# Performance work log

Measured on AMD Instinct MI355X. Metric: run time of the kernel, lower is better.

Reference implementation:

```python
import jax, jax.numpy as jnp
import numpy as np
import math

NUM_HEADS = 8
DIM = 512

def setup_inputs() -> dict:
    key = jax.random.key(0)
    ks = jax.random.split(key, 10)
    t, b, a, f, d = 32, 64, 16, 128, DIM
    inp = {
        "q_embeds": jax.random.normal(ks[0], (t, b, a, d), dtype=jnp.float32),
        "context_embeds": jax.random.normal(ks[1], (t, f, b, d), dtype=jnp.float32),
        "attn_mask": jnp.ones((b, f), dtype=jnp.int32),
        "Wq": jax.random.normal(ks[2], (d, d), dtype=jnp.float32) / math.sqrt(d),
        "bq": jnp.zeros((d,), dtype=jnp.float32),
        "Wk": jax.random.normal(ks[3], (d, d), dtype=jnp.float32) / math.sqrt(d),
        "bk": jnp.zeros((d,), dtype=jnp.float32),
        "Wv": jax.random.normal(ks[4], (d, d), dtype=jnp.float32) / math.sqrt(d),
        "bv": jnp.zeros((d,), dtype=jnp.float32),
        "Wo": jax.random.normal(ks[5], (d, d), dtype=jnp.float32) / math.sqrt(d),
        "bo": jnp.zeros((d,), dtype=jnp.float32),
    }
    return inp

def reference(q_embeds, context_embeds, attn_mask, Wq, bq, Wk, bk, Wv, bv, Wo, bo):
    t, b, a, d = q_embeds.shape
    H = NUM_HEADS
    hd = d // H
    # q: (t,b,a,d) -> (t,b,H,hd,a)
    q = (q_embeds @ Wq.T + bq).reshape(t, b, a, H, hd).transpose(0, 1, 3, 4, 2)
    f = context_embeds.shape[1]
    # video_embeds: (t,f,b,d) -> (t,b,f,d)
    video_embeds = context_embeds.transpose(0, 2, 1, 3)
    # k_proj on (t,f,b,d) then raw reshape to (t,b,f,H,hd) -- faithful to torch .reshape
    k = (context_embeds @ Wk.T + bk).reshape(t, b, f, H, hd).transpose(0, 1, 3, 2, 4)  # (t,b,H,f,hd)
    v = (video_embeds @ Wv.T + bv).reshape(t, b, f, H, hd).transpose(0, 1, 3, 4, 2)   # (t,b,H,hd,f)
    logits = (k @ q) / math.sqrt(hd)  # (t,b,H,f,a)
    mask = attn_mask[None, :, None, :, None]  # (1,b,1,f,1)
    logits = jnp.where(mask == 0, jnp.float32(-1e9), logits)
    weights = jax.nn.softmax(logits, axis=-2)  # softmax over f
    attn = v @ weights  # (t,b,H,hd,a)
    attn = attn.transpose(0, 1, 4, 2, 3).reshape(t, b, a, d)
    o = attn @ Wo.T + bo  # (t,b,a,d)
    return (o.transpose(0, 2, 1, 3), weights)
```

## Files before the change

### kernel.cpp

```cpp
#include <hip/hip_runtime.h>
#include <hip/hip_bf16.h>

typedef __attribute__((ext_vector_type(8))) short short8;
typedef __attribute__((ext_vector_type(4))) float f32x4;

#define NT 32
#define NB 64
#define NA 16
#define NF 128
#define DT 512
#define NH 8
#define NHD 64

__device__ __forceinline__ unsigned short f2b(float f) {
  return __bfloat16_as_ushort(__float2bfloat16(f));
}
__device__ __forceinline__ float b2f(unsigned short u) {
  union { unsigned u; float f; } c; c.u = ((unsigned)u) << 16;
  return c.f;
}
__device__ __forceinline__ unsigned cvt2(float a, float b) {
  return (unsigned)f2b(a) | ((unsigned)f2b(b) << 16);
}

__device__ __forceinline__ void gload16(const void* g, void* l) {
  __builtin_amdgcn_global_load_lds(
      (const __attribute__((address_space(1))) void*)g,
      (__attribute__((address_space(3))) void*)l, 16, 0, 0);
}

#define BAR() asm volatile("s_barrier" ::: "memory")

__global__ __launch_bounds__(256) void cast_kernel(const float* __restrict__ src,
                                                   unsigned short* __restrict__ dst) {
  long i = ((long)blockIdx.x * 256 + threadIdx.x) * 8;
  float4 v0 = *(const float4*)(src + i);
  float4 v1 = *(const float4*)(src + i + 4);
  uint4 o;
  o.x = cvt2(v0.x, v0.y);
  o.y = cvt2(v0.z, v0.w);
  o.z = cvt2(v1.x, v1.y);
  o.w = cvt2(v1.z, v1.w);
  *(uint4*)(dst + i) = o;
}

template <int MODE, int NCB>
__global__ __launch_bounds__(512, 4) void gemm_f32a(const float* __restrict__ A,
                                                    const unsigned short* __restrict__ Bg,
                                                    const float* __restrict__ bias0,
                                                    const float* __restrict__ bias1,
                                                    unsigned short* __restrict__ C0,
                                                    unsigned short* __restrict__ C1) {
  __shared__ __align__(16) float Asf[2][128 * 32];
  __shared__ __align__(16) unsigned short Bsb[2][256 * 32];
  const int tid = threadIdx.x;
  const int lane = tid & 63;
  const int l4 = lane & 15, lg = lane >> 4;
  const int w = tid >> 6;
  const int wm = w >> 2, wn = w & 3;

  const int nwg = gridDim.x;
  const int bid = blockIdx.x;
  const int swz = (bid & 7) * (nwg >> 3) + (bid >> 3);
  const long rowTile = swz >> NCB;
  const int colTile = swz & ((1 << NCB) - 1);

  const int sA = (tid & 7) ^ ((tid >> 3) & 7);
  const float* Agl = A + (rowTile * 128 + (tid >> 3)) * 512L + sA * 4;
  const int sB = (tid & 3) ^ ((tid >> 3) & 3);
  const unsigned short* Bgl = Bg + ((long)colTile * 256 + (tid >> 2)) * 512L + sB * 8;

  auto stage = [&](int s, int kc) {
    gload16(Agl + kc, &Asf[s][w * 256]);
    gload16(Agl + 64 * 512L + kc, &Asf[s][2048 + w * 256]);
    gload16(Bgl + kc, &Bsb[s][w * 512]);
    gload16(Bgl + 128 * 512L + kc, &Bsb[s][4096 + w * 512]);
  };

  const f32x4 zero = {0.f, 0.f, 0.f, 0.f};
  f32x4 acc[4][4];
#pragma unroll
  for (int i = 0; i < 4; i++)
#pragma unroll
    for (int j = 0; j < 4; j++) acc[i][j] = zero;

  const int chA = (l4 & 7);
  const int chB = ((l4 >> 1) & 3);

  stage(0, 0);

#pragma unroll 1
  for (int T = 0; T < 16; T++) {
    const int s = T & 1;
    BAR();
    if (T < 15) {
      stage(s ^ 1, (T + 1) * 32);
      asm volatile("s_waitcnt vmcnt(4)" ::: "memory");
    } else {
      asm volatile("s_waitcnt vmcnt(0)" ::: "memory");
    }
    BAR();
    short8 bf[4];
#pragma unroll
    for (int n = 0; n < 4; n++) {
      int rb = wn * 64 + n * 16 + l4;
      bf[n] = *(const short8*)&Bsb[s][rb * 32 + (lg ^ chB) * 8];
    }
    short8 af[4];
#pragma unroll
    for (int m = 0; m < 4; m++) {
      int ra = wm * 64 + m * 16 + l4;
      int c0 = (lg * 2) ^ chA;
      f32x4 p0 = *(const f32x4*)&Asf[s][ra * 32 + c0 * 4];
      f32x4 p1 = *(const f32x4*)&Asf[s][ra * 32 + (c0 ^ 1) * 4];
      union { unsigned u[4]; short8 s8; } cv;
      cv.u[0] = cvt2(p0[0], p0[1]);
      cv.u[1] = cvt2(p0[2], p0[3]);
      cv.u[2] = cvt2(p1[0], p1[1]);
      cv.u[3] = cvt2(p1[2], p1[3]);
      af[m] = cv.s8;
    }
    __builtin_amdgcn_s_setprio(1);
#pragma unroll
    for (int m = 0; m < 4; m++)
#pragma unroll
      for (int n = 0; n < 4; n++)
        acc[m][n] = __builtin_amdgcn_mfma_f32_16x16x32_bf16(af[m], bf[n], acc[m][n], 0, 0, 0);
    __builtin_amdgcn_s_setprio(0);
  }

  const long rowBase = rowTile * 128 + wm * 64;

  if constexpr (MODE == 0) {
    if (colTile < 2) {
#pragma unroll
      for (int n = 0; n < 4; n++) {
        int gCol = colTile * 256 + wn * 64 + n * 16 + l4;
        float bs = bias0[gCol];
#pragma unroll
        for (int m = 0; m < 4; m++)
#pragma unroll
          for (int r = 0; r < 4; r++) {
            long gRow = rowBase + m * 16 + lg * 4 + r;
            C0[gRow * 512 + gCol] = f2b(acc[m][n][r] + bs);
          }
      }
    } else {
#pragma unroll
      for (int n = 0; n < 4; n++) {
        int gCol = (colTile - 2) * 256 + wn * 64 + n * 16 + l4;
        float bs = bias1[gCol];
#pragma unroll
        for (int m = 0; m < 4; m++)
#pragma unroll
          for (int r = 0; r < 4; r++) {
            long gRow = rowBase + m * 16 + lg * 4 + r;
            long rr = gRow & 8191;
            long vrow = (gRow - rr) + ((rr & 63) << 7) + (rr >> 6);
            C1[vrow * 512 + gCol] = f2b(acc[m][n][r] + bs);
          }
      }
    }
  } else {
#pragma unroll
    for (int n = 0; n < 4; n++) {
      int gCol = colTile * 256 + wn * 64 + n * 16 + l4;
      float bs = bias0[gCol];
#pragma unroll
      for (int m = 0; m < 4; m++)
#pragma unroll
        for (int r = 0; r < 4; r++) {
          long gRow = rowBase + m * 16 + lg * 4 + r;
          C0[gRow * 512 + gCol] = f2b(acc[m][n][r] + bs);
        }
    }
  }
}

__global__ __launch_bounds__(256) void gemm_o(const unsigned short* __restrict__ A,
                                              const unsigned short* __restrict__ Bg,
                                              const float* __restrict__ bias0,
                                              float* __restrict__ C) {
  __shared__ __align__(16) unsigned short As[128 * 32];
  __shared__ __align__(16) unsigned short Bs[128 * 32];
  const int tid = threadIdx.x;
  const int lane = tid & 63;
  const int l4 = lane & 15, lg = lane >> 4;
  const int w = tid >> 6;
  const int wm = w >> 1, wn = w & 1;

  const int nwg = gridDim.x;
  const int bid = blockIdx.x;
  const int swz = (bid & 7) * (nwg >> 3) + (bid >> 3);
  const long rowTile = swz >> 2;
  const int colTile = swz & 3;

  const int srow = lane >> 2;
  const int scol = (lane & 3) * 8;
  const unsigned short* Ab = A + (rowTile * 128 + w * 16 + srow) * 512L + scol;
  const unsigned short* Ab2 = Ab + 64 * 512L;
  const unsigned short* Bb = Bg + ((long)colTile * 128 + w * 16 + srow) * 512L + scol;
  const unsigned short* Bb2 = Bb + 64 * 512L;
  unsigned short* lA = As + w * 512;
  unsigned short* lA2 = As + (w + 4) * 512;
  unsigned short* lB = Bs + w * 512;
  unsigned short* lB2 = Bs + (w + 4) * 512;

  const f32x4 zero = {0.f, 0.f, 0.f, 0.f};
  f32x4 acc[4][4];
#pragma unroll
  for (int i = 0; i < 4; i++)
#pragma unroll
    for (int j = 0; j < 4; j++) acc[i][j] = zero;

  for (int k0 = 0; k0 < 512; k0 += 32) {
    gload16(Ab + k0, lA);
    gload16(Ab2 + k0, lA2);
    gload16(Bb + k0, lB);
    gload16(Bb2 + k0, lB2);
    __syncthreads();
    short8 af[4], bfr[4];
#pragma unroll
    for (int i = 0; i < 4; i++)
      af[i] = *(const short8*)(As + (wm * 64 + i * 16 + l4) * 32 + lg * 8);
#pragma unroll
    for (int j = 0; j < 4; j++)
      bfr[j] = *(const short8*)(Bs + (wn * 64 + j * 16 + l4) * 32 + lg * 8);
#pragma unroll
    for (int i = 0; i < 4; i++)
#pragma unroll
      for (int j = 0; j < 4; j++)
        acc[i][j] = __builtin_amdgcn_mfma_f32_16x16x32_bf16(af[i], bfr[j], acc[i][j], 0, 0, 0);
    __syncthreads();
  }

  const long rowBase = rowTile * 128 + wm * 64;
#pragma unroll
  for (int j = 0; j < 4; j++) {
    int gCol = colTile * 128 + wn * 64 + j * 16 + l4;
    float bs = bias0[gCol];
#pragma unroll
    for (int i = 0; i < 4; i++)
#pragma unroll
      for (int r = 0; r < 4; r++) {
        long gRow = rowBase + i * 16 + lg * 4 + r;
        long tt = gRow >> 10;
        long bi = (gRow >> 4) & 63;
        long ai = gRow & 15;
        long orow = ((tt * 16 + ai) << 6) + bi;
        C[orow * 512 + gCol] = acc[i][j][r] + bs;
      }
  }
}

__global__ __launch_bounds__(256) void attn_kernel(const unsigned short* __restrict__ Kst,
                                                   const unsigned short* __restrict__ Vst,
                                                   const unsigned short* __restrict__ Qst,
                                                   const int* __restrict__ mask,
                                                   float* __restrict__ wout,
                                                   unsigned short* __restrict__ attn_out) {
  __shared__ __align__(16) unsigned short wt[4][16][136];
  __shared__ int msh[NF];
  const int tid = threadIdx.x;
  const int lane = tid & 63;
  const int l4 = lane & 15, lg = lane >> 4;
  const int w = tid >> 6;
  const int tb = blockIdx.x;
  const int b = tb & 63;
  if (tid < NF) msh[tid] = mask[b * NF + tid];
  __syncthreads();

  const unsigned short* Kbase = Kst + (long)tb * NF * DT;
  const unsigned short* Vbase = Vst + (long)tb * NF * DT;
  const unsigned short* Qbase = Qst + (long)tb * NA * DT;
  const f32x4 zero = {0.f, 0.f, 0.f, 0.f};

  for (int hh = 0; hh < 2; hh++) {
    const int h = w * 2 + hh;
    const int co = h * 64;
    f32x4 acc[8];
#pragma unroll
    for (int i = 0; i < 8; i++) acc[i] = zero;
#pragma unroll
    for (int ks = 0; ks < 2; ks++) {
      short8 qf = *(const short8*)(Qbase + (long)l4 * DT + co + ks * 32 + lg * 8);
#pragma unroll
      for (int m0 = 0; m0 < 8; m0++) {
        short8 kf = *(const short8*)(Kbase + (long)(m0 * 16 + l4) * DT + co + ks * 32 + lg * 8);
        acc[m0] = __builtin_amdgcn_mfma_f32_16x16x32_bf16(kf, qf, acc[m0], 0, 0, 0);
      }
    }
    float lv[8][4];
    float mx = -3.0e38f;
#pragma unroll
    for (int m0 = 0; m0 < 8; m0++)
#pragma unroll
      for (int r = 0; r < 4; r++) {
        int f = m0 * 16 + lg * 4 + r;
        float v = acc[m0][r] * 0.125f;
        if (msh[f] == 0) v = -1.0e9f;
        lv[m0][r] = v;
        mx = fmaxf(mx, v);
      }
    mx = fmaxf(mx, __shfl_xor(mx, 16, 64));
    mx = fmaxf(mx, __shfl_xor(mx, 32, 64));
    float s = 0.f;
#pragma unroll
    for (int m0 = 0; m0 < 8; m0++)
#pragma unroll
      for (int r = 0; r < 4; r++) {
        float p = __expf(lv[m0][r] - mx);
        lv[m0][r] = p;
        s += p;
      }
    s += __shfl_xor(s, 16, 64);
    s += __shfl_xor(s, 32, 64);
    float inv = 1.0f / s;
    float* wrow = wout + ((long)tb * NH + h) * (NF * NA);
#pragma unroll
    for (int m0 = 0; m0 < 8; m0++)
#pragma unroll
      for (int r = 0; r < 4; r++) {
        int f = m0 * 16 + lg * 4 + r;
        float wv = lv[m0][r] * inv;
        wrow[f * 16 + l4] = wv;
        wt[w][l4][f] = f2b(wv);
      }
    asm volatile("s_waitcnt lgkmcnt(0)" ::: "memory");
    __builtin_amdgcn_sched_barrier(0);
    f32x4 pacc[4];
#pragma unroll
    for (int m0 = 0; m0 < 4; m0++) pacc[m0] = zero;
#pragma unroll
    for (int ks = 0; ks < 4; ks++) {
      short8 wf = *(const short8*)&wt[w][l4][ks * 32 + lg * 8];
#pragma unroll
      for (int m0 = 0; m0 < 4; m0++) {
        short8 vf;
#pragma unroll
        for (int j = 0; j < 8; j++)
          vf[j] = (short)Vbase[(long)(ks * 32 + lg * 8 + j) * DT + co + m0 * 16 + l4];
        pacc[m0] = __builtin_amdgcn_mfma_f32_16x16x32_bf16(vf, wf, pacc[m0], 0, 0, 0);
      }
    }
#pragma unroll
    for (int m0 = 0; m0 < 4; m0++)
#pragma unroll
      for (int r = 0; r < 4; r++)
        attn_out[((long)tb * NA + l4) * DT + co + m0 * 16 + lg * 4 + r] = f2b(pacc[m0][r]);
  }
}

extern "C" void kernel_launch(void* const* d_in, const int* in_sizes, int n_in,
                              void* d_out, int out_size, void* d_ws, size_t ws_size,
                              hipStream_t stream) {
  const float* q_embeds = (const float*)d_in[0];
  const float* ctx = (const float*)d_in[1];
  const int* mask = (const int*)d_in[2];
  const float* Wq = (const float*)d_in[3];
  const float* bq = (const float*)d_in[4];
  const float* Wk = (const float*)d_in[5];
  const float* bk = (const float*)d_in[6];
  const float* Wv = (const float*)d_in[7];
  const float* bv = (const float*)d_in[8];
  const float* Wo = (const float*)d_in[9];
  const float* bo = (const float*)d_in[10];

  float* out0 = (float*)d_out;
  float* wout = out0 + (long)NT * NA * NB * DT;

  const long W_ELEMS = 4L * 512 * 512;
  const long MQ = (long)NT * NB * NA;
  const long MKV = (long)NT * NF * NB;
  unsigned short* Wb = (unsigned short*)d_ws;
  unsigned short* Qst = Wb + W_ELEMS;
  unsigned short* Kst = Qst + MQ * DT;
  unsigned short* Vst = Kst + MKV * DT;
  unsigned short* attnst = Vst + MKV * DT;
  size_t needed = (size_t)(W_ELEMS + 2 * MQ * DT + 2 * MKV * DT) * 2;
  if (ws_size < needed) return;

  cast_kernel<<<128, 256, 0, stream>>>(Wq, Wb);
  cast_kernel<<<128, 256, 0, stream>>>(Wk, Wb + 512 * 512);
  cast_kernel<<<128, 256, 0, stream>>>(Wv, Wb + 2 * 512 * 512);
  cast_kernel<<<128, 256, 0, stream>>>(Wo, Wb + 3 * 512 * 512);

  gemm_f32a<1, 1><<<(unsigned)(MQ / 128 * 2), 512, 0, stream>>>(
      q_embeds, Wb, bq, nullptr, Qst, nullptr);

  gemm_f32a<0, 2><<<(unsigned)(MKV / 128 * 4), 512, 0, stream>>>(
      ctx, Wb + 512 * 512, bk, bv, Kst, Vst);

  attn_kernel<<<NT * NB, 256, 0, stream>>>(Kst, Vst, Qst, mask, wout, attnst);

  gemm_o<<<(unsigned)(MQ / 128 * 4), 256, 0, stream>>>(attnst, Wb + 3 * 512 * 512, bo, out0);
}
```

Measured before the change: 796.5 us.

## Replace LDS-staged projection GEMM with direct global-to-register loads and smaller tiles

The fp32-input projection GEMM no longer stages A and B tiles through double-buffered LDS with barriers. Each lane now loads its MFMA fragments straight from global memory into registers, with no shared memory or barriers. The block shrinks from 512 threads with 128x256 tiles to 256 threads with 128x128 tiles, which doubles the grid, and the column-tile logic changes to match. This drops LDS traffic and synchronisation but loses the cross-wave reuse and prefetch overlap, so global and L2 traffic go up and load latency is exposed.

```diff
diff --git a/kernel.cpp b/kernel.cpp
--- a/kernel.cpp
+++ b/kernel.cpp
@@ -28,8 +28,6 @@
       (const __attribute__((address_space(1))) void*)g,
       (__attribute__((address_space(3))) void*)l, 16, 0, 0);
 }
-
-#define BAR() asm volatile("s_barrier" ::: "memory")
 
 __global__ __launch_bounds__(256) void cast_kernel(const float* __restrict__ src,
                                                    unsigned short* __restrict__ dst) {
@@ -45,19 +43,17 @@
 }
 
 template <int MODE, int NCB>
-__global__ __launch_bounds__(512, 4) void gemm_f32a(const float* __restrict__ A,
-                                                    const unsigned short* __restrict__ Bg,
-                                                    const float* __restrict__ bias0,
-                                                    const float* __restrict__ bias1,
-                                                    unsigned short* __restrict__ C0,
-                                                    unsigned short* __restrict__ C1) {
-  __shared__ __align__(16) float Asf[2][128 * 32];
-  __shared__ __align__(16) unsigned short Bsb[2][256 * 32];
+__global__ __launch_bounds__(256, 3) void gemm_nolds(const float* __restrict__ A,
+                                                     const unsigned short* __restrict__ Bg,
+                                                     const float* __restrict__ bias0,
+                                                     const float* __restrict__ bias1,
+                                                     unsigned short* __restrict__ C0,
+                                                     unsigned short* __restrict__ C1) {
   const int tid = threadIdx.x;
   const int lane = tid & 63;
   const int l4 = lane & 15, lg = lane >> 4;
   const int w = tid >> 6;
-  const int wm = w >> 2, wn = w & 3;
+  const int wm = w >> 1, wn = w & 1;
 
   const int nwg = gridDim.x;
   const int bid = blockIdx.x;
@@ -65,17 +61,14 @@
   const long rowTile = swz >> NCB;
   const int colTile = swz & ((1 << NCB) - 1);
 
-  const int sA = (tid & 7) ^ ((tid >> 3) & 7);
-  const float* Agl = A + (rowTile * 128 + (tid >> 3)) * 512L + sA * 4;
-  const int sB = (tid & 3) ^ ((tid >> 3) & 3);
-  const unsigned short* Bgl = Bg + ((long)colTile * 256 + (tid >> 2)) * 512L + sB * 8;
-
-  auto stage = [&](int s, int kc) {
-    gload16(Agl + kc, &Asf[s][w * 256]);
-    gload16(Agl + 64 * 512L + kc, &Asf[s][2048 + w * 256]);
-    gload16(Bgl + kc, &Bsb[s][w * 512]);
-    gload16(Bgl + 128 * 512L + kc, &Bsb[s][4096 + w * 512]);
-  };
+  const float* ap[4];
+#pragma unroll
+  for (int m = 0; m < 4; m++)
+    ap[m] = A + (rowTile * 128 + wm * 64 + m * 16 + l4) * 512L + lg * 8;
+  const unsigned short* bp[4];
+#pragma unroll
+  for (int n = 0; n < 4; n++)
+    bp[n] = Bg + ((long)colTile * 128 + wn * 64 + n * 16 + l4) * 512L + lg * 8;
 
   const f32x4 zero = {0.f, 0.f, 0.f, 0.f};
   f32x4 acc[4][4];
@@ -84,58 +77,41 @@
 #pragma unroll
     for (int j = 0; j < 4; j++) acc[i][j] = zero;
 
-  const int chA = (l4 & 7);
-  const int chB = ((l4 >> 1) & 3);
-
-  stage(0, 0);
-
 #pragma unroll 1
   for (int T = 0; T < 16; T++) {
-    const int s = T & 1;
-    BAR();
-    if (T < 15) {
-      stage(s ^ 1, (T + 1) * 32);
-      asm volatile("s_waitcnt vmcnt(4)" ::: "memory");
-    } else {
-      asm volatile("s_waitcnt vmcnt(0)" ::: "memory");
-    }
-    BAR();
+    float4 a0[4], a1[4];
     short8 bf[4];
 #pragma unroll
-    for (int n = 0; n < 4; n++) {
-      int rb = wn * 64 + n * 16 + l4;
-      bf[n] = *(const short8*)&Bsb[s][rb * 32 + (lg ^ chB) * 8];
-    }
+    for (int m = 0; m < 4; m++) {
+      a0[m] = *(const float4*)(ap[m] + T * 32);
+      a1[m] = *(const float4*)(ap[m] + T * 32 + 4);
+    }
+#pragma unroll
+    for (int n = 0; n < 4; n++) bf[n] = *(const short8*)(bp[n] + T * 32);
     short8 af[4];
 #pragma unroll
     for (int m = 0; m < 4; m++) {
-      int ra = wm * 64 + m * 16 + l4;
-      int c0 = (lg * 2) ^ chA;
-      f32x4 p0 = *(const f32x4*)&Asf[s][ra * 32 + c0 * 4];
-      f32x4 p1 = *(const f32x4*)&Asf[s][ra * 32 + (c0 ^ 1) * 4];
       union { unsigned u[4]; short8 s8; } cv;
-      cv.u[0] = cvt2(p0[0], p0[1]);
-      cv.u[1] = cvt2(p0[2], p0[3]);
-      cv.u[2] = cvt2(p1[0], p1[1]);
-      cv.u[3] = cvt2(p1[2], p1[3]);
+      cv.u[0] = cvt2(a0[m].x, a0[m].y);
+      cv.u[1] = cvt2(a0[m].z, a0[m].w);
+      cv.u[2] = cvt2(a1[m].x, a1[m].y);
+      cv.u[3] = cvt2(a1[m].z, a1[m].w);
       af[m] = cv.s8;
     }
-    __builtin_amdgcn_s_setprio(1);
 #pragma unroll
     for (int m = 0; m < 4; m++)
 #pragma unroll
       for (int n = 0; n < 4; n++)
         acc[m][n] = __builtin_amdgcn_mfma_f32_16x16x32_bf16(af[m], bf[n], acc[m][n], 0, 0, 0);
-    __builtin_amdgcn_s_setprio(0);
   }
 
   const long rowBase = rowTile * 128 + wm * 64;
 
   if constexpr (MODE == 0) {
-    if (colTile < 2) {
+    if (colTile < 4) {
 #pragma unroll
       for (int n = 0; n < 4; n++) {
-        int gCol = colTile * 256 + wn * 64 + n * 16 + l4;
+        int gCol = colTile * 128 + wn * 64 + n * 16 + l4;
         float bs = bias0[gCol];
 #pragma unroll
         for (int m = 0; m < 4; m++)
@@ -148,7 +124,7 @@
     } else {
 #pragma unroll
       for (int n = 0; n < 4; n++) {
-        int gCol = (colTile - 2) * 256 + wn * 64 + n * 16 + l4;
+        int gCol = (colTile - 4) * 128 + wn * 64 + n * 16 + l4;
         float bs = bias1[gCol];
 #pragma unroll
         for (int m = 0; m < 4; m++)
@@ -164,7 +140,7 @@
   } else {
 #pragma unroll
     for (int n = 0; n < 4; n++) {
-      int gCol = colTile * 256 + wn * 64 + n * 16 + l4;
+      int gCol = colTile * 128 + wn * 64 + n * 16 + l4;
       float bs = bias0[gCol];
 #pragma unroll
       for (int m = 0; m < 4; m++)
@@ -385,10 +361,10 @@
   cast_kernel<<<128, 256, 0, stream>>>(Wv, Wb + 2 * 512 * 512);
   cast_kernel<<<128, 256, 0, stream>>>(Wo, Wb + 3 * 512 * 512);
 
-  gemm_f32a<1, 1><<<(unsigned)(MQ / 128 * 2), 512, 0, stream>>>(
+  gemm_nolds<1, 2><<<(unsigned)(MQ / 128 * 4), 256, 0, stream>>>(
       q_embeds, Wb, bq, nullptr, Qst, nullptr);
 
-  gemm_f32a<0, 2><<<(unsigned)(MKV / 128 * 4), 512, 0, stream>>>(
+  gemm_nolds<0, 3><<<(unsigned)(MKV / 128 * 8), 256, 0, stream>>>(
       ctx, Wb + 512 * 512, bk, bv, Kst, Vst);
 
   attn_kernel<<<NT * NB, 256, 0, stream>>>(Kst, Vst, Qst, mask, wout, attnst);
```

Result: slower. 1.728 ms (+116.9%).
